# Optimization experiments

Measured on AMD Instinct MI355X. Metric: run time of the kernel, lower is better.

The kernel has to match this reference:

```python
import jax, jax.numpy as jnp
import numpy as np

E = 1024   # embed_dim
H = 16     # num_heads
DH = E // H
FF = 4096  # intermediate_size
EPS = 1e-5


def layernorm(x, g, b):
    mu = jnp.mean(x, axis=-1, keepdims=True)
    var = jnp.var(x, axis=-1, keepdims=True)
    return (x - mu) * jax.lax.rsqrt(var + EPS) * g + b


def setup_inputs() -> dict:
    key = jax.random.key(0)
    ks = jax.random.split(key, 16)
    s = 0.02
    return {
        "x": jax.random.normal(ks[0], (2, 2048, E), dtype=jnp.float32),
        "ln1_g": jnp.ones((E,), jnp.float32),
        "ln1_b": jnp.zeros((E,), jnp.float32),
        "ln2_g": jnp.ones((E,), jnp.float32),
        "ln2_b": jnp.zeros((E,), jnp.float32),
        # per-head Q/K/V projections stacked: [H, E, DH]
        "wq": jax.random.normal(ks[1], (H, E, DH), jnp.float32) * s,
        "bq": jnp.zeros((H, DH), jnp.float32),
        "wk": jax.random.normal(ks[2], (H, E, DH), jnp.float32) * s,
        "bk": jnp.zeros((H, DH), jnp.float32),
        "wv": jax.random.normal(ks[3], (H, E, DH), jnp.float32) * s,
        "bv": jnp.zeros((H, DH), jnp.float32),
        "wo": jax.random.normal(ks[4], (E, E), jnp.float32) * s,
        "bo": jnp.zeros((E,), jnp.float32),
        "w1": jax.random.normal(ks[5], (E, FF), jnp.float32) * s,
        "b1": jnp.zeros((FF,), jnp.float32),
        "w2": jax.random.normal(ks[6], (FF, E), jnp.float32) * s,
        "b2": jnp.zeros((E,), jnp.float32),
    }


def reference(x, ln1_g, ln1_b, ln2_g, ln2_b, wq, bq, wk, bk, wv, bv,
              wo, bo, w1, b1, w2, b2):
    # --- multi-head attention (pre-LN) ---
    h = layernorm(x, ln1_g, ln1_b)                       # [B,S,E]
    q = jnp.einsum('bse,hed->bhsd', h, wq) + bq[:, None, :]
    k = jnp.einsum('bse,hed->bhsd', h, wk) + bk[:, None, :]
    v = jnp.einsum('bse,hed->bhsd', h, wv) + bv[:, None, :]
    scores = jnp.einsum('bhsd,bhtd->bhst', q, k) / jnp.sqrt(
        jnp.asarray(DH, x.dtype))                        # [B,H,S,S]
    w = jax.nn.softmax(scores, axis=-1)
    attn = jnp.einsum('bhst,bhtd->bhsd', w, v)           # [B,H,S,DH]
    B, _, S, _ = attn.shape
    concat = attn.transpose(0, 2, 1, 3).reshape(B, S, E)  # head concat order
    x = x + concat @ wo + bo
    # --- feed-forward (pre-LN), exact GELU, dropout_p=0 ---
    h2 = layernorm(x, ln2_g, ln2_b)
    ff = jax.nn.gelu(h2 @ w1 + b1, approximate=False) @ w2 + b2
    return x + ff
```

## Files before the change

### kernel.cpp

```cpp
#include <hip/hip_runtime.h>
#include <hip/hip_bf16.h>
#include <math.h>

typedef __attribute__((ext_vector_type(8))) short short8;
typedef __attribute__((ext_vector_type(4))) float f32x4;
typedef __attribute__((ext_vector_type(16))) float f32x16;
typedef __attribute__((ext_vector_type(4))) unsigned u32x4;

#define MFMA_BF16(a, b, c) __builtin_amdgcn_mfma_f32_16x16x32_bf16(a, b, c, 0, 0, 0)
#define MFMA32_BF16(a, b, c) __builtin_amdgcn_mfma_f32_32x32x16_bf16(a, b, c, 0, 0, 0)
#define BAR() __builtin_amdgcn_s_barrier()

#define GLD_LDS16(g, l)                                              \
  __builtin_amdgcn_global_load_lds(                                  \
      (const __attribute__((address_space(1))) void*)(g),            \
      (__attribute__((address_space(3))) void*)(l), 16, 0, 0)

template <int N>
__device__ __forceinline__ void waitcnt_vm() {
  if constexpr (N == 0) asm volatile("s_waitcnt vmcnt(0)" ::: "memory");
  else if constexpr (N == 2) asm volatile("s_waitcnt vmcnt(2)" ::: "memory");
  else if constexpr (N == 4) asm volatile("s_waitcnt vmcnt(4)" ::: "memory");
  else if constexpr (N == 6) asm volatile("s_waitcnt vmcnt(6)" ::: "memory");
  else if constexpr (N == 8) asm volatile("s_waitcnt vmcnt(8)" ::: "memory");
}

__device__ __forceinline__ unsigned cvt_pk_bf16(float lo, float hi) {
  unsigned r;
  asm("v_cvt_pk_bf16_f32 %0, %1, %2" : "=v"(r) : "v"(lo), "v"(hi));
  return r;
}
#define PSWAP(a, b) asm volatile("v_permlane32_swap_b32 %0, %1" : "+v"(a), "+v"(b))

__device__ __forceinline__ unsigned short f2bf(float f) {
  union { float f; unsigned u; } v; v.f = f;
  unsigned r = v.u + 0x7FFFu + ((v.u >> 16) & 1u);
  return (unsigned short)(r >> 16);
}
__device__ __forceinline__ float bf2f(unsigned short u) {
  union { unsigned u; float f; } v; v.u = ((unsigned)u) << 16;
  return v.f;
}

__global__ __launch_bounds__(256) void transpose_cast(
    const float* __restrict__ in, unsigned short* __restrict__ out,
    int R, int C, size_t in_bs, size_t out_bs) {
  __shared__ float t[32][33];
  const float* inp = in + blockIdx.z * in_bs;
  unsigned short* outp = out + blockIdx.z * out_bs;
  const int c0 = blockIdx.x * 32, r0 = blockIdx.y * 32;
  const int tx = threadIdx.x, ty = threadIdx.y;
#pragma unroll
  for (int i = 0; i < 32; i += 8)
    t[ty + i][tx] = inp[(size_t)(r0 + ty + i) * C + c0 + tx];
  __syncthreads();
#pragma unroll
  for (int i = 0; i < 32; i += 8)
    outp[(size_t)(c0 + ty + i) * R + r0 + tx] = f2bf(t[tx][ty + i]);
}

__global__ void concat_bias(const float* __restrict__ bq, const float* __restrict__ bk,
                            const float* __restrict__ bv, float* __restrict__ bcat) {
  int i = blockIdx.x * 256 + threadIdx.x;
  if (i < 1024) bcat[i] = bq[i];
  else if (i < 2048) bcat[i] = bk[i - 1024];
  else if (i < 3072) bcat[i] = bv[i - 2048];
}

__global__ __launch_bounds__(512) void vtrans(
    const unsigned short* __restrict__ qkv, unsigned short* __restrict__ vt) {
  __shared__ unsigned short t[64][65];
  const int bh = blockIdx.y;
  const int s0 = blockIdx.x * 64;
  const int tx = threadIdx.x;
  const int ty = threadIdx.y;
  const unsigned short* in =
      qkv + (size_t)(bh >> 4) * 2048 * 3072 + 2048 + (bh & 15) * 64;
#pragma unroll
  for (int i = 0; i < 8; ++i)
    t[ty * 8 + i][tx] = in[(size_t)(s0 + ty * 8 + i) * 3072 + tx];
  __syncthreads();
  unsigned short* o = vt + (size_t)bh * 64 * 2048 + s0;
#pragma unroll
  for (int i = 0; i < 8; ++i)
    o[(size_t)(ty * 8 + i) * 2048 + tx] = t[tx][ty * 8 + i];
}

__global__ __launch_bounds__(256) void ln_kernel(
    const float* __restrict__ x, const float* __restrict__ g,
    const float* __restrict__ bb, unsigned short* __restrict__ out) {
  const int row = blockIdx.x, tid = threadIdx.x;
  const float4 v = ((const float4*)(x + (size_t)row * 1024))[tid];
  float s = v.x + v.y + v.z + v.w;
  float ss = v.x * v.x + v.y * v.y + v.z * v.z + v.w * v.w;
#pragma unroll
  for (int k = 1; k < 64; k <<= 1) {
    s += __shfl_xor(s, k, 64);
    ss += __shfl_xor(ss, k, 64);
  }
  __shared__ float red[8];
  const int wid = tid >> 6;
  if ((tid & 63) == 0) { red[wid] = s; red[wid + 4] = ss; }
  __syncthreads();
  s = red[0] + red[1] + red[2] + red[3];
  ss = red[4] + red[5] + red[6] + red[7];
  const float mu = s * (1.0f / 1024.0f);
  const float var = ss * (1.0f / 1024.0f) - mu * mu;
  const float rs = rsqrtf(var + 1e-5f);
  const float4 gv = ((const float4*)g)[tid];
  const float4 bv = ((const float4*)bb)[tid];
  ushort4 o;
  o.x = f2bf((v.x - mu) * rs * gv.x + bv.x);
  o.y = f2bf((v.y - mu) * rs * gv.y + bv.y);
  o.z = f2bf((v.z - mu) * rs * gv.z + bv.z);
  o.w = f2bf((v.w - mu) * rs * gv.w + bv.w);
  ((ushort4*)(out + (size_t)row * 1024))[tid] = o;
}

template <int QM, int QN>
__device__ __forceinline__ void mfq(f32x4 (&acc)[8][4], short8 (&af)[4][2],
                                    short8 (&bf)[2][2]) {
  __builtin_amdgcn_s_setprio(1);
#pragma unroll
  for (int i = 0; i < 4; ++i)
#pragma unroll
    for (int nf = 0; nf < 2; ++nf) {
      acc[QM * 4 + i][QN * 2 + nf] =
          MFMA_BF16(af[i][0], bf[nf][0], acc[QM * 4 + i][QN * 2 + nf]);
      acc[QM * 4 + i][QN * 2 + nf] =
          MFMA_BF16(af[i][1], bf[nf][1], acc[QM * 4 + i][QN * 2 + nf]);
    }
  __builtin_amdgcn_s_setprio(0);
}

template <int EPI>
__global__ __launch_bounds__(512, 2) void gemm256(
    const unsigned short* __restrict__ A, const unsigned short* __restrict__ Bt,
    const float* __restrict__ bias, void* __restrict__ Cout,
    int M, int N, int K) {
  extern __shared__ unsigned short L[];
  const int tid = threadIdx.x;
  const int wv = tid >> 6, lane = tid & 63;
  const int li = lane & 15, gi = lane >> 4;
  const int wm = wv >> 2, wn = wv & 3;
  const int bm = blockIdx.y, bn = blockIdx.x;
  const size_t Ksz = (size_t)K;
  const int KT = K >> 6;

  auto lds = [&](int buf, int op, int half) -> unsigned short* {
    return L + (size_t)(((buf * 2 + op) * 2 + half)) * 8192;
  };

  const int sr8 = tid >> 3;
  const int segG = (tid & 7) ^ (sr8 & 7);
  const unsigned short* Ag = A + (size_t)(bm * 256 + sr8) * Ksz + segG * 8;
  const unsigned short* Bg = Bt + (size_t)(bn * 256 + sr8) * Ksz + segG * 8;
  const int wbase = wv * 512;

  auto stg = [&](int buf, int op, int half, int tile) {
    const unsigned short* g =
        (op ? Bg : Ag) + (size_t)(half * 128) * Ksz + (tile % KT) * 64;
    unsigned short* d = lds(buf, op, half);
    GLD_LDS16(g, d + wbase);
    GLD_LDS16(g + (size_t)64 * Ksz, d + 4096 + wbase);
  };

  f32x4 acc[8][4];
#pragma unroll
  for (int m = 0; m < 8; ++m)
#pragma unroll
    for (int n = 0; n < 4; ++n) acc[m][n] = (f32x4)0.0f;

  short8 af[4][2], b0[2][2], b1[2][2];
  auto ldA = [&](int buf, int qm) {
    const unsigned short* p = lds(buf, 0, wm);
#pragma unroll
    for (int i = 0; i < 4; ++i) {
      const int r = qm * 64 + i * 16 + li;
#pragma unroll
      for (int kk = 0; kk < 2; ++kk)
        af[i][kk] = *(const short8*)(p + r * 64 + (((kk * 4 + gi) ^ (r & 7)) * 8));
    }
  };
  auto ldB = [&](short8 (&bf)[2][2], int buf, int qn) {
    const unsigned short* p = lds(buf, 1, wn >> 1);
#pragma unroll
    for (int nf = 0; nf < 2; ++nf) {
      const int r = (wn & 1) * 64 + qn * 32 + nf * 16 + li;
#pragma unroll
      for (int kk = 0; kk < 2; ++kk)
        bf[nf][kk] = *(const short8*)(p + r * 64 + (((kk * 4 + gi) ^ (r & 7)) * 8));
    }
  };

  stg(0, 0, 0, 0); stg(0, 0, 1, 0); stg(0, 1, 0, 0); stg(0, 1, 1, 0);
  stg(1, 0, 0, 1);

  for (int j = 0; j < KT / 2; ++j) {
    const int t1 = 2 * j + 1, t2 = 2 * j + 2, t3 = 2 * j + 3;
    waitcnt_vm<2>(); BAR();
    ldA(0, 0); ldB(b0, 0, 0);
    stg(1, 0, 1, t1); stg(1, 1, 0, t1);
    BAR(); mfq<0, 0>(acc, af, b0); BAR();
    ldB(b1, 0, 1);
    stg(1, 1, 1, t1);
    BAR(); mfq<0, 1>(acc, af, b1); BAR();
    ldA(0, 1);
    stg(0, 0, 0, t2);
    BAR(); mfq<1, 0>(acc, af, b0); BAR();
    mfq<1, 1>(acc, af, b1); BAR();
    waitcnt_vm<2>(); BAR();
    ldA(1, 0); ldB(b0, 1, 0);
    stg(0, 0, 1, t2); stg(0, 1, 0, t2);
    BAR(); mfq<0, 0>(acc, af, b0); BAR();
    ldB(b1, 1, 1);
    stg(0, 1, 1, t2);
    BAR(); mfq<0, 1>(acc, af, b1); BAR();
    ldA(1, 1);
    stg(1, 0, 0, t3);
    BAR(); mfq<1, 0>(acc, af, b0); BAR();
    mfq<1, 1>(acc, af, b1); BAR();
  }

  const int row0 = bm * 256 + wm * 128 + gi * 4;
  const int col0 = bn * 256 + wn * 64 + li;
#pragma unroll
  for (int mf = 0; mf < 8; ++mf) {
#pragma unroll
    for (int nf = 0; nf < 4; ++nf) {
      const int col = col0 + nf * 16;
      const float bi = bias[col];
#pragma unroll
      for (int r = 0; r < 4; ++r) {
        const int row = row0 + mf * 16 + r;
        float v = acc[mf][nf][r] + bi;
        if (EPI == 2) v = 0.5f * v * (1.0f + erff(v * 0.70710678118654752f));
        ((unsigned short*)Cout)[(size_t)row * N + col] = f2bf(v);
      }
    }
  }
}

template <int EPI, int BN>
__global__ __launch_bounds__(256, (BN == 128) ? 2 : 3) void gemm_bt(
    const unsigned short* __restrict__ A, const unsigned short* __restrict__ Bt,
    const float* __restrict__ bias, const float* __restrict__ res,
    void* __restrict__ Cout, int M, int N, int K) {
  constexpr int NFR = BN / 32;
  constexpr int BISS = BN / 32;
  constexpr int ISS = 4 + BISS;
  __shared__ unsigned short As[2][128 * 64];
  __shared__ unsigned short Bs[2][BN * 64];
  const int tid = threadIdx.x;
  const int wid = tid >> 6, lane = tid & 63;
  const int li = lane & 15, gi = lane >> 4;
  const int bm = blockIdx.y, bn = blockIdx.x;
  const int wr = (wid >> 1) << 6;
  const int wc = (wid & 1) * (BN / 2);

  f32x4 acc[4][NFR];
#pragma unroll
  for (int m = 0; m < 4; ++m)
#pragma unroll
    for (int n = 0; n < NFR; ++n) acc[m][n] = (f32x4)0.0f;

  const size_t Ksz = (size_t)K;
  const int srow = tid >> 3;
  const int segG = (tid & 7) ^ (srow & 7);
  const unsigned short* Ab = A + (size_t)(bm * 128 + srow) * Ksz + segG * 8;
  const unsigned short* Bb = Bt + (size_t)(bn * BN + srow) * Ksz + segG * 8;

  auto stage = [&](int buf, int kt) {
#pragma unroll
    for (int c = 0; c < 4; ++c)
      GLD_LDS16(Ab + (size_t)(c * 32) * Ksz + kt, &As[buf][c * 2048 + wid * 512]);
#pragma unroll
    for (int c = 0; c < BISS; ++c)
      GLD_LDS16(Bb + (size_t)(c * 32) * Ksz + kt, &Bs[buf][c * 2048 + wid * 512]);
  };

  auto compute = [&](int ib) {
    const unsigned short* As_ = As[ib];
    const unsigned short* Bs_ = Bs[ib];
    short8 af[4][2], bf[NFR][2];
#pragma unroll
    for (int m = 0; m < 4; ++m)
#pragma unroll
      for (int kk = 0; kk < 2; ++kk) {
        const int row = wr + m * 16 + li;
        af[m][kk] = *(const short8*)(As_ + row * 64 + ((kk * 4 + gi) ^ (row & 7)) * 8);
      }
#pragma unroll
    for (int n = 0; n < NFR; ++n)
#pragma unroll
      for (int kk = 0; kk < 2; ++kk) {
        const int row = wc + n * 16 + li;
        bf[n][kk] = *(const short8*)(Bs_ + row * 64 + ((kk * 4 + gi) ^ (row & 7)) * 8);
      }
    __builtin_amdgcn_s_setprio(1);
#pragma unroll
    for (int m = 0; m < 4; ++m)
#pragma unroll
      for (int n = 0; n < NFR; ++n) {
        acc[m][n] = MFMA_BF16(af[m][0], bf[n][0], acc[m][n]);
        acc[m][n] = MFMA_BF16(af[m][1], bf[n][1], acc[m][n]);
      }
    __builtin_amdgcn_s_setprio(0);
  };

  const int KT = K >> 6;
  stage(0, 0);
  for (int i = 0; i < KT - 1; ++i) {
    stage((i + 1) & 1, (i + 1) << 6);
    waitcnt_vm<ISS>();
    __builtin_amdgcn_s_barrier();
    __builtin_amdgcn_sched_barrier(0);
    compute(i & 1);
    __builtin_amdgcn_s_barrier();
  }
  waitcnt_vm<0>();
  __builtin_amdgcn_s_barrier();
  __builtin_amdgcn_sched_barrier(0);
  compute((KT - 1) & 1);

  const int row_base = bm * 128 + wr + gi * 4;
  const int col_base = bn * BN + wc + li;
#pragma unroll
  for (int m = 0; m < 4; ++m) {
#pragma unroll
    for (int n = 0; n < NFR; ++n) {
      const int col = col_base + n * 16;
      const float bi = bias[col];
#pragma unroll
      for (int r = 0; r < 4; ++r) {
        const int row = row_base + m * 16 + r;
        float v = acc[m][n][r] + bi;
        if (EPI == 2) v = 0.5f * v * (1.0f + erff(v * 0.70710678118654752f));
        const size_t idx = (size_t)row * N + col;
        if (EPI == 1) ((float*)Cout)[idx] = v + res[idx];
        else ((unsigned short*)Cout)[idx] = f2bf(v);
      }
    }
  }
}

__global__ __launch_bounds__(256, 4) void attn_kernel(
    const unsigned short* __restrict__ qkv, const unsigned short* __restrict__ vt,
    unsigned short* __restrict__ op0, unsigned short* __restrict__ op1,
    float* __restrict__ lpart) {
  __shared__ unsigned short Kl[2][4096];
  __shared__ unsigned short Vl[2][4096];
  const int tid = threadIdx.x;
  const int wid = tid >> 6, lane = tid & 63;
  const int l31 = lane & 31, hiq = lane >> 5;
  const int kvh = blockIdx.z & 1, b = blockIdx.z >> 1, h = blockIdx.y;
  const int q0 = blockIdx.x * 128 + wid * 32;
  const int LD = 3072;
  const size_t base = (size_t)b * 2048 * LD;
  const size_t kvoff = (size_t)kvh * 1024 * LD;

  short8 qb[4];
  {
    const unsigned short* qp = qkv + base + (size_t)(q0 + l31) * LD + h * 64 + hiq * 8;
#pragma unroll
    for (int ds = 0; ds < 4; ++ds) qb[ds] = *(const short8*)(qp + ds * 16);
  }

  f32x16 o0 = (f32x16)0.0f, o1 = (f32x16)0.0f;
  float la = 0.0f, lb = 0.0f;

  const int rw = lane >> 3;
  const int sgG = (lane & 7) ^ rw;
  const unsigned short* kdma = qkv + base + kvoff + 1024 + h * 64 + sgG * 8 +
                               (size_t)(wid * 16 + rw) * LD;
  const unsigned short* vdma = vt + (size_t)(b * 16 + h) * 64 * 2048 +
                               (size_t)(wid * 16 + rw) * 2048 + kvh * 1024 + sgG * 8;

  auto kstage = [&](int buf, int t) {
    GLD_LDS16(kdma + (size_t)t * 64 * LD, &Kl[buf][wid * 1024]);
    GLD_LDS16(kdma + (size_t)(t * 64 + 8) * LD, &Kl[buf][wid * 1024 + 512]);
  };
  auto vstage = [&](int buf, int t) {
    GLD_LDS16(vdma + t * 64, &Vl[buf][wid * 1024]);
    GLD_LDS16(vdma + 8 * 2048 + t * 64, &Vl[buf][wid * 1024 + 512]);
  };

  auto compute = [&](int ib) {
    const unsigned short* kl = Kl[ib];
    const unsigned short* vl = Vl[ib];
    short8 kf[2][4];
#pragma unroll
    for (int kvb = 0; kvb < 2; ++kvb)
#pragma unroll
      for (int ds = 0; ds < 4; ++ds)
        kf[kvb][ds] = *(const short8*)(
            kl + (kvb * 32 + l31) * 64 + (((2 * ds + hiq) ^ (l31 & 7)) * 8));

    f32x16 sA = (f32x16)0.0f, sB = (f32x16)0.0f;
    __builtin_amdgcn_s_setprio(1);
#pragma unroll
    for (int ds = 0; ds < 4; ++ds) {
      sA = MFMA32_BF16(kf[0][ds], qb[ds], sA);
      sB = MFMA32_BF16(kf[1][ds], qb[ds], sB);
    }
    __builtin_amdgcn_s_setprio(0);

#pragma unroll
    for (int kvb = 0; kvb < 2; ++kvb) {
      const f32x16 s = kvb ? sB : sA;
      unsigned P[8];
#pragma unroll
      for (int i = 0; i < 8; ++i) {
        const float pe = __expf(s[2 * i] * 0.125f);
        const float po = __expf(s[2 * i + 1] * 0.125f);
        la += pe; lb += po;
        P[i] = cvt_pk_bf16(pe, po);
      }
      PSWAP(P[0], P[2]); PSWAP(P[1], P[3]);
      PSWAP(P[4], P[6]); PSWAP(P[5], P[7]);
      const short8 pa0 = __builtin_bit_cast(short8, (u32x4){P[0], P[1], P[2], P[3]});
      const short8 pa1 = __builtin_bit_cast(short8, (u32x4){P[4], P[5], P[6], P[7]});
      const int sg0 = 4 * kvb + hiq, sg1 = 4 * kvb + 2 + hiq;
      const short8 v00 = *(const short8*)(vl + l31 * 64 + ((sg0 ^ (l31 & 7)) * 8));
      const short8 v01 = *(const short8*)(vl + l31 * 64 + ((sg1 ^ (l31 & 7)) * 8));
      const short8 v10 = *(const short8*)(vl + (32 + l31) * 64 + ((sg0 ^ (l31 & 7)) * 8));
      const short8 v11 = *(const short8*)(vl + (32 + l31) * 64 + ((sg1 ^ (l31 & 7)) * 8));
      __builtin_amdgcn_s_setprio(1);
      o0 = MFMA32_BF16(pa0, v00, o0);
      o0 = MFMA32_BF16(pa1, v01, o0);
      o1 = MFMA32_BF16(pa0, v10, o1);
      o1 = MFMA32_BF16(pa1, v11, o1);
      __builtin_amdgcn_s_setprio(0);
    }
  };

  kstage(0, 0);
  vstage(0, 0);
  for (int t = 0; t < 15; ++t) {
    kstage((t + 1) & 1, t + 1);
    vstage((t + 1) & 1, t + 1);
    waitcnt_vm<4>();
    __builtin_amdgcn_s_barrier();
    __builtin_amdgcn_sched_barrier(0);
    compute(t & 1);
    __builtin_amdgcn_s_barrier();
  }
  waitcnt_vm<0>();
  __builtin_amdgcn_s_barrier();
  __builtin_amdgcn_sched_barrier(0);
  compute(15 & 1);

  const float lsum = la + lb;
  const float lt = lsum + __shfl_xor(lsum, 32, 64);
  if (hiq == 0)
    lpart[(size_t)kvh * 65536 + ((size_t)(b * 2048 + q0 + l31) * 16) + h] = lt;

  unsigned short* op = kvh ? op1 : op0;
#pragma unroll
  for (int r = 0; r < 16; ++r) {
    const int crow = (r & 3) + 8 * (r >> 2) + 4 * hiq;
    const size_t rowb = (size_t)(b * 2048 + q0 + crow) * 1024 + h * 64 + l31;
    op[rowb]      = f2bf(o0[r]);
    op[rowb + 32] = f2bf(o1[r]);
  }
}

__global__ __launch_bounds__(256) void attn_combine(
    const unsigned short* __restrict__ op0, unsigned short* __restrict__ op1io,
    const float* __restrict__ lpart) {
  const size_t i8 = (size_t)blockIdx.x * 256 + threadIdx.x;
  const size_t g = (i8 * 8) >> 6;
  const float inv = 1.0f / (lpart[g] + lpart[g + 65536]);
  const short8 a = *(const short8*)(op0 + i8 * 8);
  const short8 c = *(const short8*)(op1io + i8 * 8);
  short8 o;
#pragma unroll
  for (int j = 0; j < 8; ++j)
    o[j] = (short)f2bf((bf2f((unsigned short)a[j]) + bf2f((unsigned short)c[j])) * inv);
  *(short8*)(op1io + i8 * 8) = o;
}

extern "C" void kernel_launch(void* const* d_in, const int* in_sizes, int n_in,
                              void* d_out, int out_size, void* d_ws, size_t ws_size,
                              hipStream_t stream) {
  const float* x     = (const float*)d_in[0];
  const float* ln1_g = (const float*)d_in[1];
  const float* ln1_b = (const float*)d_in[2];
  const float* ln2_g = (const float*)d_in[3];
  const float* ln2_b = (const float*)d_in[4];
  const float* wq    = (const float*)d_in[5];
  const float* bq    = (const float*)d_in[6];
  const float* wk    = (const float*)d_in[7];
  const float* bk    = (const float*)d_in[8];
  const float* wv    = (const float*)d_in[9];
  const float* bv    = (const float*)d_in[10];
  const float* wo    = (const float*)d_in[11];
  const float* bo    = (const float*)d_in[12];
  const float* w1    = (const float*)d_in[13];
  const float* b1    = (const float*)d_in[14];
  const float* w2    = (const float*)d_in[15];
  const float* b2    = (const float*)d_in[16];
  float* out = (float*)d_out;

  hipFuncSetAttribute((const void*)gemm256<0>,
                      hipFuncAttributeMaxDynamicSharedMemorySize, 131072);
  hipFuncSetAttribute((const void*)gemm256<2>,
                      hipFuncAttributeMaxDynamicSharedMemorySize, 131072);

  char* p = (char*)d_ws;
  unsigned short* ws_h     = (unsigned short*)p; p += 4096ull * 1024 * 2;
  unsigned short* ws_qkv   = (unsigned short*)p; p += 4096ull * 3072 * 2;
  unsigned short* ws_attn  = (unsigned short*)p; p += 4096ull * 1024 * 2;
  unsigned short* ws_wqkvT = (unsigned short*)p; p += 3072ull * 1024 * 2;
  unsigned short* ws_woT   = (unsigned short*)p; p += 1024ull * 1024 * 2;
  unsigned short* ws_w1T   = (unsigned short*)p; p += 4096ull * 1024 * 2;
  unsigned short* ws_w2T   = (unsigned short*)p; p += 1024ull * 4096 * 2;
  float*          ws_bqkv  = (float*)p;          p += 3072 * 4;
  float*          ws_l     = (float*)p;          p += 2ull * 65536 * 4;
  unsigned short* ws_ff = ws_qkv;
  unsigned short* ws_vt = ws_w1T;

  const dim3 tb(32, 8);
  transpose_cast<<<dim3(2, 32, 16), tb, 0, stream>>>(
      wq, ws_wqkvT, 1024, 64, (size_t)(1024 * 64), (size_t)(64 * 1024));
  transpose_cast<<<dim3(2, 32, 16), tb, 0, stream>>>(
      wk, ws_wqkvT + 1024ull * 1024, 1024, 64, (size_t)(1024 * 64), (size_t)(64 * 1024));
  transpose_cast<<<dim3(2, 32, 16), tb, 0, stream>>>(
      wv, ws_wqkvT + 2048ull * 1024, 1024, 64, (size_t)(1024 * 64), (size_t)(64 * 1024));
  transpose_cast<<<dim3(32, 32, 1), tb, 0, stream>>>(wo, ws_woT, 1024, 1024, 0, 0);
  concat_bias<<<12, 256, 0, stream>>>(bq, bk, bv, ws_bqkv);

  ln_kernel<<<4096, 256, 0, stream>>>(x, ln1_g, ln1_b, ws_h);
  gemm256<0><<<dim3(12, 16), 512, 131072, stream>>>(ws_h, ws_wqkvT, ws_bqkv,
                                                    ws_qkv, 4096, 3072, 1024);
  vtrans<<<dim3(32, 32), dim3(64, 8), 0, stream>>>(ws_qkv, ws_vt);
  attn_kernel<<<dim3(16, 16, 4), 256, 0, stream>>>(ws_qkv, ws_vt, ws_h, ws_attn, ws_l);
  attn_combine<<<2048, 256, 0, stream>>>(ws_h, ws_attn, ws_l);
  transpose_cast<<<dim3(128, 32, 1), tb, 0, stream>>>(w1, ws_w1T, 1024, 4096, 0, 0);
  transpose_cast<<<dim3(32, 128, 1), tb, 0, stream>>>(w2, ws_w2T, 4096, 1024, 0, 0);
  gemm_bt<1, 64><<<dim3(16, 32), 256, 0, stream>>>(ws_attn, ws_woT, bo, x,
                                                   out, 4096, 1024, 1024);
  ln_kernel<<<4096, 256, 0, stream>>>(out, ln2_g, ln2_b, ws_h);
  gemm256<2><<<dim3(16, 16), 512, 131072, stream>>>(ws_h, ws_w1T, b1,
                                                    ws_ff, 4096, 4096, 1024);
  gemm_bt<1, 64><<<dim3(16, 32), 256, 0, stream>>>(ws_ff, ws_w2T, b2, out,
                                                   out, 4096, 1024, 4096);
}
```

Measured before the change: 252.6 us.

## Run FFN down-projection as split-K 256x256 GEMM with combine kernel

The FFN second GEMM now uses the large 256x256 tiled kernel with a 4-way K split via gridDim.z. Each split writes bf16 partials into reused workspace buffers. A new combine kernel sums the partials, adds the bias and accumulates into the residual output. This trades extra partial-sum memory traffic and bf16 rounding of partials for a more efficient tile shape and better occupancy.

```diff
diff --git a/kernel.cpp b/kernel.cpp
--- a/kernel.cpp
+++ b/kernel.cpp
@@ -137,7 +137,9 @@
 __global__ __launch_bounds__(512, 2) void gemm256(
     const unsigned short* __restrict__ A, const unsigned short* __restrict__ Bt,
     const float* __restrict__ bias, void* __restrict__ Cout,
-    int M, int N, int K) {
+    int M, int N, int K,
+    unsigned short* __restrict__ p0, unsigned short* __restrict__ p1,
+    unsigned short* __restrict__ p2, unsigned short* __restrict__ p3) {
   extern __shared__ unsigned short L[];
   const int tid = threadIdx.x;
   const int wv = tid >> 6, lane = tid & 63;
@@ -145,7 +147,8 @@
   const int wm = wv >> 2, wn = wv & 3;
   const int bm = blockIdx.y, bn = blockIdx.x;
   const size_t Ksz = (size_t)K;
-  const int KT = K >> 6;
+  const int KTloc = (K / (int)gridDim.z) >> 6;
+  const int k0 = blockIdx.z * (KTloc << 6);
 
   auto lds = [&](int buf, int op, int half) -> unsigned short* {
     return L + (size_t)(((buf * 2 + op) * 2 + half)) * 8192;
@@ -153,13 +156,13 @@
 
   const int sr8 = tid >> 3;
   const int segG = (tid & 7) ^ (sr8 & 7);
-  const unsigned short* Ag = A + (size_t)(bm * 256 + sr8) * Ksz + segG * 8;
-  const unsigned short* Bg = Bt + (size_t)(bn * 256 + sr8) * Ksz + segG * 8;
+  const unsigned short* Ag = A + (size_t)(bm * 256 + sr8) * Ksz + segG * 8 + k0;
+  const unsigned short* Bg = Bt + (size_t)(bn * 256 + sr8) * Ksz + segG * 8 + k0;
   const int wbase = wv * 512;
 
   auto stg = [&](int buf, int op, int half, int tile) {
     const unsigned short* g =
-        (op ? Bg : Ag) + (size_t)(half * 128) * Ksz + (tile % KT) * 64;
+        (op ? Bg : Ag) + (size_t)(half * 128) * Ksz + (tile % KTloc) * 64;
     unsigned short* d = lds(buf, op, half);
     GLD_LDS16(g, d + wbase);
     GLD_LDS16(g + (size_t)64 * Ksz, d + 4096 + wbase);
@@ -196,7 +199,7 @@
   stg(0, 0, 0, 0); stg(0, 0, 1, 0); stg(0, 1, 0, 0); stg(0, 1, 1, 0);
   stg(1, 0, 0, 1);
 
-  for (int j = 0; j < KT / 2; ++j) {
+  for (int j = 0; j < KTloc / 2; ++j) {
     const int t1 = 2 * j + 1, t2 = 2 * j + 2, t3 = 2 * j + 3;
     waitcnt_vm<2>(); BAR();
     ldA(0, 0); ldB(b0, 0, 0);
@@ -222,6 +225,10 @@
     mfq<1, 1>(acc, af, b1); BAR();
   }
 
+  unsigned short* Pz =
+      (EPI == 3) ? ((blockIdx.z == 0) ? p0 : (blockIdx.z == 1) ? p1
+                    : (blockIdx.z == 2) ? p2 : p3)
+                 : (unsigned short*)Cout;
   const int row0 = bm * 256 + wm * 128 + gi * 4;
   const int col0 = bn * 256 + wn * 64 + li;
 #pragma unroll
@@ -229,16 +236,40 @@
 #pragma unroll
     for (int nf = 0; nf < 4; ++nf) {
       const int col = col0 + nf * 16;
-      const float bi = bias[col];
+      const float bi = (EPI == 3) ? 0.0f : bias[col];
 #pragma unroll
       for (int r = 0; r < 4; ++r) {
         const int row = row0 + mf * 16 + r;
         float v = acc[mf][nf][r] + bi;
         if (EPI == 2) v = 0.5f * v * (1.0f + erff(v * 0.70710678118654752f));
-        ((unsigned short*)Cout)[(size_t)row * N + col] = f2bf(v);
+        Pz[(size_t)row * N + col] = f2bf(v);
       }
     }
   }
+}
+
+__global__ __launch_bounds__(256) void ffn2_combine(
+    const unsigned short* __restrict__ p0, const unsigned short* __restrict__ p1,
+    const unsigned short* __restrict__ p2, const unsigned short* __restrict__ p3,
+    const float* __restrict__ b2, float* __restrict__ out) {
+  const size_t i8 = (size_t)blockIdx.x * 256 + threadIdx.x;
+  const size_t e0 = i8 * 8;
+  const int col = (int)(e0 & 1023);
+  const short8 a0 = *(const short8*)(p0 + e0);
+  const short8 a1 = *(const short8*)(p1 + e0);
+  const short8 a2 = *(const short8*)(p2 + e0);
+  const short8 a3 = *(const short8*)(p3 + e0);
+  float4 o0 = ((float4*)out)[i8 * 2];
+  float4 o1 = ((float4*)out)[i8 * 2 + 1];
+  float v[8];
+#pragma unroll
+  for (int j = 0; j < 8; ++j)
+    v[j] = bf2f((unsigned short)a0[j]) + bf2f((unsigned short)a1[j]) +
+           bf2f((unsigned short)a2[j]) + bf2f((unsigned short)a3[j]) + b2[col + j];
+  o0.x += v[0]; o0.y += v[1]; o0.z += v[2]; o0.w += v[3];
+  o1.x += v[4]; o1.y += v[5]; o1.z += v[6]; o1.w += v[7];
+  ((float4*)out)[i8 * 2] = o0;
+  ((float4*)out)[i8 * 2 + 1] = o1;
 }
 
 template <int EPI, int BN>
@@ -506,6 +537,8 @@
                       hipFuncAttributeMaxDynamicSharedMemorySize, 131072);
   hipFuncSetAttribute((const void*)gemm256<2>,
                       hipFuncAttributeMaxDynamicSharedMemorySize, 131072);
+  hipFuncSetAttribute((const void*)gemm256<3>,
+                      hipFuncAttributeMaxDynamicSharedMemorySize, 131072);
 
   char* p = (char*)d_ws;
   unsigned short* ws_h     = (unsigned short*)p; p += 4096ull * 1024 * 2;
@@ -519,6 +552,10 @@
   float*          ws_l     = (float*)p;          p += 2ull * 65536 * 4;
   unsigned short* ws_ff = ws_qkv;
   unsigned short* ws_vt = ws_w1T;
+  unsigned short* ws_p0 = ws_h;
+  unsigned short* ws_p1 = ws_attn;
+  unsigned short* ws_p2 = ws_wqkvT;
+  unsigned short* ws_p3 = ws_w1T;
 
   const dim3 tb(32, 8);
   transpose_cast<<<dim3(2, 32, 16), tb, 0, stream>>>(
@@ -531,8 +568,9 @@
   concat_bias<<<12, 256, 0, stream>>>(bq, bk, bv, ws_bqkv);
 
   ln_kernel<<<4096, 256, 0, stream>>>(x, ln1_g, ln1_b, ws_h);
-  gemm256<0><<<dim3(12, 16), 512, 131072, stream>>>(ws_h, ws_wqkvT, ws_bqkv,
-                                                    ws_qkv, 4096, 3072, 1024);
+  gemm256<0><<<dim3(12, 16, 1), 512, 131072, stream>>>(
+      ws_h, ws_wqkvT, ws_bqkv, ws_qkv, 4096, 3072, 1024,
+      nullptr, nullptr, nullptr, nullptr);
   vtrans<<<dim3(32, 32), dim3(64, 8), 0, stream>>>(ws_qkv, ws_vt);
   attn_kernel<<<dim3(16, 16, 4), 256, 0, stream>>>(ws_qkv, ws_vt, ws_h, ws_attn, ws_l);
   attn_combine<<<2048, 256, 0, stream>>>(ws_h, ws_attn, ws_l);
@@ -541,8 +579,11 @@
   gemm_bt<1, 64><<<dim3(16, 32), 256, 0, stream>>>(ws_attn, ws_woT, bo, x,
                                                    out, 4096, 1024, 1024);
   ln_kernel<<<4096, 256, 0, stream>>>(out, ln2_g, ln2_b, ws_h);
-  gemm256<2><<<dim3(16, 16), 512, 131072, stream>>>(ws_h, ws_w1T, b1,
-                                                    ws_ff, 4096, 4096, 1024);
-  gemm_bt<1, 64><<<dim3(16, 32), 256, 0, stream>>>(ws_ff, ws_w2T, b2, out,
-                                                   out, 4096, 1024, 4096);
-}
+  gemm256<2><<<dim3(16, 16, 1), 512, 131072, stream>>>(
+      ws_h, ws_w1T, b1, ws_ff, 4096, 4096, 1024,
+      nullptr, nullptr, nullptr, nullptr);
+  gemm256<3><<<dim3(4, 16, 4), 512, 131072, stream>>>(
+      ws_ff, ws_w2T, nullptr, nullptr, 4096, 1024, 4096,
+      ws_p0, ws_p1, ws_p2, ws_p3);
+  ffn2_combine<<<2048, 256, 0, stream>>>(ws_p0, ws_p1, ws_p2, ws_p3, b2, out);
+}
```

Measured after the change: 244.3 us. 3.3% less time.
